# Kernel tuning notes

Hardware: AMD Instinct MI355X
Metric: run time of the kernel (lower is better)

The kernel has to match this reference:

```python
import jax, jax.numpy as jnp
import numpy as np

B, S, D, F, E, K = 2, 1024, 2048, 1024, 8, 2


def setup_inputs() -> dict:
    key = jax.random.key(0)
    ks = jax.random.split(key, 5)
    scale_x = 0.02
    return {
        "x": jax.random.normal(ks[0], (B, S, D), dtype=jnp.float32),
        "w_router": jax.random.normal(ks[1], (E, D), dtype=jnp.float32) * scale_x,
        "w_gate": jax.random.normal(ks[2], (E, F, D), dtype=jnp.float32) * scale_x,
        "w_up": jax.random.normal(ks[3], (E, F, D), dtype=jnp.float32) * scale_x,
        "w_down": jax.random.normal(ks[4], (E, D, F), dtype=jnp.float32) * scale_x,
        "top_k": K,
    }


def reference(x, w_router, w_gate, w_up, w_down, top_k):
    # Router: logits [B,S,E] -> top-k indices + softmax over top-k logits (fp32)
    logits = jnp.einsum("bsd,ed->bse", x, w_router)
    top_logits, top_idx = jax.lax.top_k(logits, top_k)          # [B,S,K]
    gates = jax.nn.softmax(top_logits.astype(jnp.float32), axis=-1)
    # SwitchGLU: per-expert gated MLP. Compute all experts densely, then gather
    # the selected expert output per token (reference-faithful math).
    h = jax.nn.silu(jnp.einsum("bsd,efd->besf", x, w_gate)) * jnp.einsum(
        "bsd,efd->besf", x, w_up
    )                                                            # [B,E,S,F]
    out_all = jnp.einsum("besf,edf->bsed", h, w_down)            # [B,S,E,D]
    y = jnp.take_along_axis(out_all, top_idx[..., None], axis=2)  # [B,S,K,D]
    return (y * gates[..., None].astype(y.dtype)).sum(axis=-2)   # [B,S,D]
```

## Files before the change

### kernel.cpp

```cpp
#include <hip/hip_runtime.h>
#include <hip/hip_bf16.h>

#define T_TOK 2048
#define DIM   2048
#define FFN   1024
#define NE    8

typedef __attribute__((ext_vector_type(8))) short bf16x8;
typedef __attribute__((ext_vector_type(4))) float f32x4;

__device__ __forceinline__ unsigned short f2bf(float f) {
  __hip_bfloat16 h = __float2bfloat16(f);
  return __builtin_bit_cast(unsigned short, h);
}

__device__ __forceinline__ void gload_lds16(const unsigned short* g, unsigned short* l) {
  __builtin_amdgcn_global_load_lds(
      (const __attribute__((address_space(1))) void*)g,
      (__attribute__((address_space(3))) void*)l, 16, 0, 0);
}

#define XN4 (T_TOK * DIM / 4)
#define WN4 (NE * FFN * DIM / 4)
__global__ void cvt_all(const float* __restrict__ x, const float* __restrict__ wg,
                        const float* __restrict__ wu, const float* __restrict__ wd,
                        unsigned short* __restrict__ xb, unsigned short* __restrict__ wgb,
                        unsigned short* __restrict__ wub, unsigned short* __restrict__ wdb) {
  long i = (long)blockIdx.x * blockDim.x + threadIdx.x;
  long stride = (long)gridDim.x * blockDim.x;
  const long TOTAL = (long)XN4 + 3L * WN4;
  for (; i < TOTAL; i += stride) {
    const float4* src; ushort4* dst; long j;
    if (i < XN4) {
      src = reinterpret_cast<const float4*>(x); dst = reinterpret_cast<ushort4*>(xb); j = i;
    } else {
      long k = i - XN4; int seg = (int)(k >> 22); j = k & (WN4 - 1);
      src = reinterpret_cast<const float4*>(seg == 0 ? wg : (seg == 1 ? wu : wd));
      dst = reinterpret_cast<ushort4*>(seg == 0 ? wgb : (seg == 1 ? wub : wdb));
    }
    float4 v = src[j];
    ushort4 o;
    o.x = f2bf(v.x); o.y = f2bf(v.y); o.z = f2bf(v.z); o.w = f2bf(v.w);
    dst[j] = o;
  }
}

__global__ __launch_bounds__(256) void router_topk(
    const float* __restrict__ x, const float* __restrict__ wr,
    int* __restrict__ top_i, float* __restrict__ top_g) {
  int t = blockIdx.x * 4 + (threadIdx.x >> 6);
  int lane = threadIdx.x & 63;
  const float4* xr = reinterpret_cast<const float4*>(x) + (size_t)t * (DIM / 4);
  const float4* wrv = reinterpret_cast<const float4*>(wr);
  float acc[NE];
#pragma unroll
  for (int e = 0; e < NE; ++e) acc[e] = 0.f;
#pragma unroll
  for (int it = 0; it < DIM / 4 / 64; ++it) {
    int d4 = it * 64 + lane;
    float4 xv = xr[d4];
#pragma unroll
    for (int e = 0; e < NE; ++e) {
      float4 wv = wrv[e * (DIM / 4) + d4];
      acc[e] += xv.x * wv.x + xv.y * wv.y + xv.z * wv.z + xv.w * wv.w;
    }
  }
#pragma unroll
  for (int off = 32; off > 0; off >>= 1) {
#pragma unroll
    for (int e = 0; e < NE; ++e) acc[e] += __shfl_xor(acc[e], off, 64);
  }
  if (lane == 0) {
    int i0 = 0; float m0 = acc[0];
#pragma unroll
    for (int e = 1; e < NE; ++e) if (acc[e] > m0) { m0 = acc[e]; i0 = e; }
    int i1 = -1; float m1 = -3.4e38f;
#pragma unroll
    for (int e = 0; e < NE; ++e) if (e != i0 && acc[e] > m1) { m1 = acc[e]; i1 = e; }
    float tv = expf(m1 - m0);
    float den = 1.f + tv;
    top_i[t * 2 + 0] = i0; top_i[t * 2 + 1] = i1;
    top_g[t * 2 + 0] = 1.f / den; top_g[t * 2 + 1] = tv / den;
  }
}

__global__ void count_offsets(const int* __restrict__ top_i,
                              int* __restrict__ offs, int* __restrict__ cursor) {
  __shared__ int cnt[NE];
  if (threadIdx.x < NE) cnt[threadIdx.x] = 0;
  __syncthreads();
  for (int i = threadIdx.x; i < T_TOK * 2; i += blockDim.x) atomicAdd(&cnt[top_i[i]], 1);
  __syncthreads();
  if (threadIdx.x == 0) {
    int s = 0;
    for (int e = 0; e < NE; ++e) { offs[e] = s; cursor[e] = s; s += cnt[e]; }
    offs[NE] = s;
  }
}

__global__ void scatter_tokens(const int* __restrict__ top_i, const float* __restrict__ top_g,
                               int* __restrict__ cursor, int* __restrict__ tok_list,
                               float* __restrict__ gate_lst, int* __restrict__ slot_lst) {
  int t = blockIdx.x * blockDim.x + threadIdx.x;
  if (t >= T_TOK) return;
#pragma unroll
  for (int s = 0; s < 2; ++s) {
    int e = top_i[t * 2 + s];
    int p = atomicAdd(&cursor[e], 1);
    tok_list[p] = t;
    gate_lst[p] = top_g[t * 2 + s];
    slot_lst[p] = s;
  }
}

__global__ __launch_bounds__(256, 4) void gateup_gemm(
    const unsigned short* __restrict__ xb, const unsigned short* __restrict__ wgb,
    const unsigned short* __restrict__ wub, const int* __restrict__ tok_list,
    const int* __restrict__ offs, unsigned short* __restrict__ hbuf) {
  const int e = blockIdx.z;
  const int row0 = offs[e];
  const int n_e = offs[e + 1] - row0;
  const int mt = blockIdx.y;
  if (mt * 64 >= n_e) return;
  const int nt = blockIdx.x;

  __shared__ unsigned short As[64 * 64];
  __shared__ unsigned short Bg[64 * 64];
  __shared__ unsigned short Bu[64 * 64];

  const int tid = threadIdx.x;
  const int wid = tid >> 6;
  const int lane = tid & 63;

  const int gchunk = (((lane & 7) ^ ((lane >> 3) & 7)) << 3);

  const unsigned short* gA[2];
  int lAoff[2];
#pragma unroll
  for (int p = 0; p < 2; ++p) {
    int rt = wid * 16 + p * 8 + (lane >> 3);
    int ar = mt * 64 + rt; if (ar >= n_e) ar = n_e - 1;
    gA[p] = xb + (size_t)tok_list[row0 + ar] * DIM + gchunk;
    lAoff[p] = (wid * 16 + p * 8) * 64;
  }
  const size_t wbase = (size_t)e * FFN * DIM + (size_t)(nt * 64) * DIM;
  const unsigned short* gG[2];
  const unsigned short* gU[2];
  int lBoff[2];
#pragma unroll
  for (int p = 0; p < 2; ++p) {
    int rt = wid * 16 + p * 8 + (lane >> 3);
    gG[p] = wgb + wbase + (size_t)rt * DIM + gchunk;
    gU[p] = wub + wbase + (size_t)rt * DIM + gchunk;
    lBoff[p] = (wid * 16 + p * 8) * 64;
  }

  f32x4 accg[2][2];
  f32x4 accu[2][2];
#pragma unroll
  for (int i = 0; i < 2; ++i)
#pragma unroll
    for (int j = 0; j < 2; ++j) {
      accg[i][j] = (f32x4){0.f, 0.f, 0.f, 0.f};
      accu[i][j] = (f32x4){0.f, 0.f, 0.f, 0.f};
    }

  const int warow = (wid >> 1) * 32;
  const int wacol = (wid & 1) * 32;
  const int frow = lane & 15;
  const int eo0 = ((((lane >> 4)) ^ (lane & 7)) << 3);
  const int eo1 = (((4 + (lane >> 4)) ^ (lane & 7)) << 3);

  for (int k0 = 0; k0 < DIM; k0 += 64) {
#pragma unroll
    for (int p = 0; p < 2; ++p) {
      gload_lds16(gA[p] + k0, &As[lAoff[p]]);
      gload_lds16(gG[p] + k0, &Bg[lBoff[p]]);
      gload_lds16(gU[p] + k0, &Bu[lBoff[p]]);
    }
    __syncthreads();
#pragma unroll
    for (int kk = 0; kk < 2; ++kk) {
      const int eo = kk ? eo1 : eo0;
      bf16x8 af[2], bg[2], bu[2];
#pragma unroll
      for (int i = 0; i < 2; ++i)
        af[i] = *reinterpret_cast<const bf16x8*>(&As[(warow + i * 16 + frow) * 64 + eo]);
#pragma unroll
      for (int j = 0; j < 2; ++j) {
        bg[j] = *reinterpret_cast<const bf16x8*>(&Bg[(wacol + j * 16 + frow) * 64 + eo]);
        bu[j] = *reinterpret_cast<const bf16x8*>(&Bu[(wacol + j * 16 + frow) * 64 + eo]);
      }
#pragma unroll
      for (int i = 0; i < 2; ++i)
#pragma unroll
        for (int j = 0; j < 2; ++j) {
          accg[i][j] = __builtin_amdgcn_mfma_f32_16x16x32_bf16(af[i], bg[j], accg[i][j], 0, 0, 0);
          accu[i][j] = __builtin_amdgcn_mfma_f32_16x16x32_bf16(af[i], bu[j], accu[i][j], 0, 0, 0);
        }
    }
    __syncthreads();
  }

#pragma unroll
  for (int i = 0; i < 2; ++i) {
#pragma unroll
    for (int jj = 0; jj < 4; ++jj) {
      int r = mt * 64 + warow + i * 16 + (lane >> 4) * 4 + jj;
      if (r < n_e) {
#pragma unroll
        for (int j = 0; j < 2; ++j) {
          float g = accg[i][j][jj];
          float u = accu[i][j][jj];
          float h = (g / (1.f + __expf(-g))) * u;
          int f = nt * 64 + wacol + j * 16 + (lane & 15);
          hbuf[(size_t)(row0 + r) * FFN + f] = f2bf(h);
        }
      }
    }
  }
}

__global__ __launch_bounds__(256, 4) void down_gemm(
    const unsigned short* __restrict__ hbuf, const unsigned short* __restrict__ wdb,
    const int* __restrict__ tok_list, const float* __restrict__ gate_lst,
    const int* __restrict__ slot_lst, const int* __restrict__ offs,
    float* __restrict__ yslots) {
  const int e = blockIdx.z;
  const int row0 = offs[e];
  const int n_e = offs[e + 1] - row0;
  const int mt = blockIdx.y;
  if (mt * 64 >= n_e) return;
  const int nt = blockIdx.x;

  __shared__ unsigned short As[64 * 64];
  __shared__ unsigned short Bs[128 * 64];

  const int tid = threadIdx.x;
  const int wid = tid >> 6;
  const int lane = tid & 63;

  const int gchunk = (((lane & 7) ^ ((lane >> 3) & 7)) << 3);

  const unsigned short* gA[2];
  int lAoff[2];
#pragma unroll
  for (int p = 0; p < 2; ++p) {
    int rt = wid * 16 + p * 8 + (lane >> 3);
    int ar = mt * 64 + rt; if (ar >= n_e) ar = n_e - 1;
    gA[p] = hbuf + (size_t)(row0 + ar) * FFN + gchunk;
    lAoff[p] = (wid * 16 + p * 8) * 64;
  }
  const unsigned short* gB[4];
  int lBoff[4];
#pragma unroll
  for (int p = 0; p < 4; ++p) {
    int rt = wid * 32 + p * 8 + (lane >> 3);
    gB[p] = wdb + ((size_t)e * DIM + nt * 128 + rt) * FFN + gchunk;
    lBoff[p] = (wid * 32 + p * 8) * 64;
  }

  f32x4 acc[2][4];
#pragma unroll
  for (int i = 0; i < 2; ++i)
#pragma unroll
    for (int j = 0; j < 4; ++j) acc[i][j] = (f32x4){0.f, 0.f, 0.f, 0.f};

  const int warow = (wid >> 1) * 32;
  const int wacol = (wid & 1) * 64;
  const int frow = lane & 15;
  const int eo0 = ((((lane >> 4)) ^ (lane & 7)) << 3);
  const int eo1 = (((4 + (lane >> 4)) ^ (lane & 7)) << 3);

  for (int k0 = 0; k0 < FFN; k0 += 64) {
#pragma unroll
    for (int p = 0; p < 2; ++p) gload_lds16(gA[p] + k0, &As[lAoff[p]]);
#pragma unroll
    for (int p = 0; p < 4; ++p) gload_lds16(gB[p] + k0, &Bs[lBoff[p]]);
    __syncthreads();
#pragma unroll
    for (int kk = 0; kk < 2; ++kk) {
      const int eo = kk ? eo1 : eo0;
      bf16x8 af[2], bf[4];
#pragma unroll
      for (int i = 0; i < 2; ++i)
        af[i] = *reinterpret_cast<const bf16x8*>(&As[(warow + i * 16 + frow) * 64 + eo]);
#pragma unroll
      for (int j = 0; j < 4; ++j)
        bf[j] = *reinterpret_cast<const bf16x8*>(&Bs[(wacol + j * 16 + frow) * 64 + eo]);
#pragma unroll
      for (int i = 0; i < 2; ++i)
#pragma unroll
        for (int j = 0; j < 4; ++j)
          acc[i][j] = __builtin_amdgcn_mfma_f32_16x16x32_bf16(af[i], bf[j], acc[i][j], 0, 0, 0);
    }
    __syncthreads();
  }

#pragma unroll
  for (int i = 0; i < 2; ++i) {
#pragma unroll
    for (int jj = 0; jj < 4; ++jj) {
      int r = mt * 64 + warow + i * 16 + (lane >> 4) * 4 + jj;
      if (r < n_e) {
        int tk = tok_list[row0 + r];
        float gt = gate_lst[row0 + r];
        int sl = slot_lst[row0 + r];
        float* yrow = yslots + ((size_t)sl * T_TOK + tk) * DIM;
#pragma unroll
        for (int j = 0; j < 4; ++j) {
          int d = nt * 128 + wacol + j * 16 + (lane & 15);
          yrow[d] = gt * acc[i][j][jj];
        }
      }
    }
  }
}

__global__ void combine(const float* __restrict__ y, float* __restrict__ out) {
  int i = blockIdx.x * blockDim.x + threadIdx.x;
  int stride = gridDim.x * blockDim.x;
  const float4* y0 = reinterpret_cast<const float4*>(y);
  const float4* y1 = reinterpret_cast<const float4*>(y + (size_t)T_TOK * DIM);
  float4* o = reinterpret_cast<float4*>(out);
  for (; i < T_TOK * DIM / 4; i += stride) {
    float4 a = y0[i], b = y1[i];
    float4 r;
    r.x = a.x + b.x; r.y = a.y + b.y; r.z = a.z + b.z; r.w = a.w + b.w;
    o[i] = r;
  }
}

extern "C" void kernel_launch(void* const* d_in, const int* in_sizes, int n_in,
                              void* d_out, int out_size, void* d_ws, size_t ws_size,
                              hipStream_t stream) {
  const float* x = (const float*)d_in[0];
  const float* wr = (const float*)d_in[1];
  const float* wg = (const float*)d_in[2];
  const float* wu = (const float*)d_in[3];
  const float* wd = (const float*)d_in[4];
  float* out = (float*)d_out;

  char* ws = (char*)d_ws;
  size_t off = 0;
  auto alloc = [&](size_t bytes) {
    char* p = ws + off;
    off += (bytes + 255) & ~(size_t)255;
    return p;
  };
  unsigned short* xb   = (unsigned short*)alloc((size_t)T_TOK * DIM * 2);
  unsigned short* wgb  = (unsigned short*)alloc((size_t)NE * FFN * DIM * 2);
  unsigned short* wub  = (unsigned short*)alloc((size_t)NE * FFN * DIM * 2);
  unsigned short* wdb  = (unsigned short*)alloc((size_t)NE * DIM * FFN * 2);
  unsigned short* hbuf = (unsigned short*)alloc((size_t)T_TOK * 2 * FFN * 2);
  float* yslots        = (float*)alloc((size_t)2 * T_TOK * DIM * 4);
  int* top_i     = (int*)alloc(T_TOK * 2 * 4);
  float* top_g   = (float*)alloc(T_TOK * 2 * 4);
  int* tok_list  = (int*)alloc(T_TOK * 2 * 4);
  float* gate_lst = (float*)alloc(T_TOK * 2 * 4);
  int* slot_lst  = (int*)alloc(T_TOK * 2 * 4);
  int* offs      = (int*)alloc(64);
  int* cursor    = (int*)alloc(64);
  if (off > ws_size) return;

  cvt_all<<<4096, 256, 0, stream>>>(x, wg, wu, wd, xb, wgb, wub, wdb);
  router_topk<<<T_TOK / 4, 256, 0, stream>>>(x, wr, top_i, top_g);
  count_offsets<<<1, 256, 0, stream>>>(top_i, offs, cursor);
  scatter_tokens<<<(T_TOK + 255) / 256, 256, 0, stream>>>(top_i, top_g, cursor, tok_list,
                                                          gate_lst, slot_lst);
  gateup_gemm<<<dim3(FFN / 64, 32, NE), 256, 0, stream>>>(xb, wgb, wub, tok_list, offs, hbuf);
  down_gemm<<<dim3(DIM / 128, 32, NE), 256, 0, stream>>>(hbuf, wdb, tok_list, gate_lst,
                                                         slot_lst, offs, yslots);
  combine<<<2048, 256, 0, stream>>>(yslots, out);
}
```

Baseline: 199.8 us.

## Overlap down-proj weight conversion with gate/up GEMM and widen fp32-to-bf16 stores

Replaces the single fused conversion kernel with per-tensor conversion kernels that write 8 bf16 values per thread per step. The conversion of w_down is moved into extra blocks of the gate/up GEMM grid, so it runs at the same time as the GEMM instead of before it. This aims to hide part of the memory-bound weight conversion behind compute. The risk is that the extra blocks compete with GEMM blocks for bandwidth and CU slots.

After: 221.6 us. 1.11x slower.

```diff
diff --git a/kernel.cpp b/kernel.cpp
--- a/kernel.cpp
+++ b/kernel.cpp
@@ -7,6 +7,7 @@
 #define NE    8
 
 typedef __attribute__((ext_vector_type(8))) short bf16x8;
+typedef __attribute__((ext_vector_type(8))) unsigned short u16x8;
 typedef __attribute__((ext_vector_type(4))) float f32x4;
 
 __device__ __forceinline__ unsigned short f2bf(float f) {
@@ -20,28 +21,25 @@
       (__attribute__((address_space(3))) void*)l, 16, 0, 0);
 }
 
-#define XN4 (T_TOK * DIM / 4)
-#define WN4 (NE * FFN * DIM / 4)
-__global__ void cvt_all(const float* __restrict__ x, const float* __restrict__ wg,
-                        const float* __restrict__ wu, const float* __restrict__ wd,
-                        unsigned short* __restrict__ xb, unsigned short* __restrict__ wgb,
-                        unsigned short* __restrict__ wub, unsigned short* __restrict__ wdb) {
-  long i = (long)blockIdx.x * blockDim.x + threadIdx.x;
-  long stride = (long)gridDim.x * blockDim.x;
-  const long TOTAL = (long)XN4 + 3L * WN4;
-  for (; i < TOTAL; i += stride) {
-    const float4* src; ushort4* dst; long j;
-    if (i < XN4) {
-      src = reinterpret_cast<const float4*>(x); dst = reinterpret_cast<ushort4*>(xb); j = i;
-    } else {
-      long k = i - XN4; int seg = (int)(k >> 22); j = k & (WN4 - 1);
-      src = reinterpret_cast<const float4*>(seg == 0 ? wg : (seg == 1 ? wu : wd));
-      dst = reinterpret_cast<ushort4*>(seg == 0 ? wgb : (seg == 1 ? wub : wdb));
-    }
-    float4 v = src[j];
-    ushort4 o;
-    o.x = f2bf(v.x); o.y = f2bf(v.y); o.z = f2bf(v.z); o.w = f2bf(v.w);
-    dst[j] = o;
+__device__ __forceinline__ u16x8 cvt8(float4 a, float4 b) {
+  u16x8 o;
+  o[0] = f2bf(a.x); o[1] = f2bf(a.y); o[2] = f2bf(a.z); o[3] = f2bf(a.w);
+  o[4] = f2bf(b.x); o[5] = f2bf(b.y); o[6] = f2bf(b.z); o[7] = f2bf(b.w);
+  return o;
+}
+
+__global__ __launch_bounds__(256) void cvt4(const float* __restrict__ src,
+                                            unsigned short* __restrict__ dst) {
+  const int tid = blockIdx.x * 256 + threadIdx.x;
+  const int nthreads = gridDim.x * 256;
+  const float4* s = reinterpret_cast<const float4*>(src);
+  u16x8* d = reinterpret_cast<u16x8*>(dst);
+#pragma unroll
+  for (int g = 0; g < 4; ++g) {
+    long grp = (long)g * nthreads + tid;
+    float4 a = s[grp * 2];
+    float4 b = s[grp * 2 + 1];
+    d[grp] = cvt8(a, b);
   }
 }
 
@@ -116,7 +114,22 @@
 __global__ __launch_bounds__(256, 4) void gateup_gemm(
     const unsigned short* __restrict__ xb, const unsigned short* __restrict__ wgb,
     const unsigned short* __restrict__ wub, const int* __restrict__ tok_list,
-    const int* __restrict__ offs, unsigned short* __restrict__ hbuf) {
+    const int* __restrict__ offs, unsigned short* __restrict__ hbuf,
+    const float* __restrict__ wd_f32, unsigned short* __restrict__ wdb) {
+  if (blockIdx.x >= FFN / 64) {
+    int cb = (blockIdx.x - FFN / 64) + 4 * (blockIdx.y + 32 * blockIdx.z);
+    int t = cb * 256 + threadIdx.x;
+    const float4* s = reinterpret_cast<const float4*>(wd_f32);
+    u16x8* d = reinterpret_cast<u16x8*>(wdb);
+#pragma unroll
+    for (int g = 0; g < 8; ++g) {
+      long grp = (long)g * 262144 + t;
+      float4 a = s[grp * 2];
+      float4 b = s[grp * 2 + 1];
+      d[grp] = cvt8(a, b);
+    }
+    return;
+  }
   const int e = blockIdx.z;
   const int row0 = offs[e];
   const int n_e = offs[e + 1] - row0;
@@ -363,12 +376,15 @@
   int* cursor    = (int*)alloc(64);
   if (off > ws_size) return;
 
-  cvt_all<<<4096, 256, 0, stream>>>(x, wg, wu, wd, xb, wgb, wub, wdb);
+  cvt4<<<512, 256, 0, stream>>>(x, xb);
+  cvt4<<<2048, 256, 0, stream>>>(wg, wgb);
+  cvt4<<<2048, 256, 0, stream>>>(wu, wub);
   router_topk<<<T_TOK / 4, 256, 0, stream>>>(x, wr, top_i, top_g);
   count_offsets<<<1, 256, 0, stream>>>(top_i, offs, cursor);
   scatter_tokens<<<(T_TOK + 255) / 256, 256, 0, stream>>>(top_i, top_g, cursor, tok_list,
                                                           gate_lst, slot_lst);
-  gateup_gemm<<<dim3(FFN / 64, 32, NE), 256, 0, stream>>>(xb, wgb, wub, tok_list, offs, hbuf);
+  gateup_gemm<<<dim3(FFN / 64 + 4, 32, NE), 256, 0, stream>>>(xb, wgb, wub, tok_list, offs,
+                                                              hbuf, wd, wdb);
   down_gemm<<<dim3(DIM / 128, 32, NE), 256, 0, stream>>>(hbuf, wdb, tok_list, gate_lst,
                                                          slot_lst, offs, yslots);
   combine<<<2048, 256, 0, stream>>>(yslots, out);
```

## Fuse x bf16 conversion into router, atomic-accumulate down output, drop combine

Applied to the files above, without the earlier changes.

The activation fp32-to-bf16 conversion moves into the router kernel, which already reads x, and weight conversion becomes its own kernel with a fixed per-block layout. The down GEMM now atomically adds gated results straight into a zeroed output, so the 32 MB two-slot scratch buffer, the slot list and the combine kernel all go away. This cuts global memory traffic and one launch. In exchange it adds a zeroing pass and float atomics, which make the summation order of the two expert contributions nondeterministic.

Measured after the change: 211.8 us. 6.0% more time.

```diff
diff --git a/kernel.cpp b/kernel.cpp
--- a/kernel.cpp
+++ b/kernel.cpp
@@ -20,38 +20,44 @@
       (__attribute__((address_space(3))) void*)l, 16, 0, 0);
 }
 
-#define XN4 (T_TOK * DIM / 4)
-#define WN4 (NE * FFN * DIM / 4)
-__global__ void cvt_all(const float* __restrict__ x, const float* __restrict__ wg,
-                        const float* __restrict__ wu, const float* __restrict__ wd,
-                        unsigned short* __restrict__ xb, unsigned short* __restrict__ wgb,
-                        unsigned short* __restrict__ wub, unsigned short* __restrict__ wdb) {
-  long i = (long)blockIdx.x * blockDim.x + threadIdx.x;
-  long stride = (long)gridDim.x * blockDim.x;
-  const long TOTAL = (long)XN4 + 3L * WN4;
-  for (; i < TOTAL; i += stride) {
-    const float4* src; ushort4* dst; long j;
-    if (i < XN4) {
-      src = reinterpret_cast<const float4*>(x); dst = reinterpret_cast<ushort4*>(xb); j = i;
-    } else {
-      long k = i - XN4; int seg = (int)(k >> 22); j = k & (WN4 - 1);
-      src = reinterpret_cast<const float4*>(seg == 0 ? wg : (seg == 1 ? wu : wd));
-      dst = reinterpret_cast<ushort4*>(seg == 0 ? wgb : (seg == 1 ? wub : wdb));
-    }
-    float4 v = src[j];
+__global__ void zero_out(float4* __restrict__ o, int n4) {
+  int i = blockIdx.x * blockDim.x + threadIdx.x;
+  int stride = gridDim.x * blockDim.x;
+  float4 z = {0.f, 0.f, 0.f, 0.f};
+  for (; i < n4; i += stride) o[i] = z;
+}
+
+__global__ __launch_bounds__(256) void cvt_w(
+    const float* __restrict__ wg, const float* __restrict__ wu, const float* __restrict__ wd,
+    unsigned short* __restrict__ wgb, unsigned short* __restrict__ wub,
+    unsigned short* __restrict__ wdb) {
+  int b = blockIdx.x;
+  const float* src; unsigned short* dst;
+  if (b < 4096)       { src = wg; dst = wgb; }
+  else if (b < 8192)  { src = wu; dst = wub; b -= 4096; }
+  else                { src = wd; dst = wdb; b -= 8192; }
+  const float4* s = reinterpret_cast<const float4*>(src);
+  ushort4* d = reinterpret_cast<ushort4*>(dst);
+  long base = (long)b * 1024 + threadIdx.x;
+#pragma unroll
+  for (int g = 0; g < 4; ++g) {
+    long i = base + g * 256;
+    float4 v = s[i];
     ushort4 o;
     o.x = f2bf(v.x); o.y = f2bf(v.y); o.z = f2bf(v.z); o.w = f2bf(v.w);
-    dst[j] = o;
+    d[i] = o;
   }
 }
 
 __global__ __launch_bounds__(256) void router_topk(
     const float* __restrict__ x, const float* __restrict__ wr,
-    int* __restrict__ top_i, float* __restrict__ top_g) {
+    int* __restrict__ top_i, float* __restrict__ top_g,
+    unsigned short* __restrict__ xb) {
   int t = blockIdx.x * 4 + (threadIdx.x >> 6);
   int lane = threadIdx.x & 63;
   const float4* xr = reinterpret_cast<const float4*>(x) + (size_t)t * (DIM / 4);
   const float4* wrv = reinterpret_cast<const float4*>(wr);
+  ushort4* xbr = reinterpret_cast<ushort4*>(xb + (size_t)t * DIM);
   float acc[NE];
 #pragma unroll
   for (int e = 0; e < NE; ++e) acc[e] = 0.f;
@@ -59,6 +65,9 @@
   for (int it = 0; it < DIM / 4 / 64; ++it) {
     int d4 = it * 64 + lane;
     float4 xv = xr[d4];
+    ushort4 o;
+    o.x = f2bf(xv.x); o.y = f2bf(xv.y); o.z = f2bf(xv.z); o.w = f2bf(xv.w);
+    xbr[d4] = o;
 #pragma unroll
     for (int e = 0; e < NE; ++e) {
       float4 wv = wrv[e * (DIM / 4) + d4];
@@ -100,7 +109,7 @@
 
 __global__ void scatter_tokens(const int* __restrict__ top_i, const float* __restrict__ top_g,
                                int* __restrict__ cursor, int* __restrict__ tok_list,
-                               float* __restrict__ gate_lst, int* __restrict__ slot_lst) {
+                               float* __restrict__ gate_lst) {
   int t = blockIdx.x * blockDim.x + threadIdx.x;
   if (t >= T_TOK) return;
 #pragma unroll
@@ -109,7 +118,6 @@
     int p = atomicAdd(&cursor[e], 1);
     tok_list[p] = t;
     gate_lst[p] = top_g[t * 2 + s];
-    slot_lst[p] = s;
   }
 }
 
@@ -224,8 +232,7 @@
 __global__ __launch_bounds__(256, 4) void down_gemm(
     const unsigned short* __restrict__ hbuf, const unsigned short* __restrict__ wdb,
     const int* __restrict__ tok_list, const float* __restrict__ gate_lst,
-    const int* __restrict__ slot_lst, const int* __restrict__ offs,
-    float* __restrict__ yslots) {
+    const int* __restrict__ offs, float* __restrict__ out) {
   const int e = blockIdx.z;
   const int row0 = offs[e];
   const int n_e = offs[e + 1] - row0;
@@ -305,29 +312,14 @@
       if (r < n_e) {
         int tk = tok_list[row0 + r];
         float gt = gate_lst[row0 + r];
-        int sl = slot_lst[row0 + r];
-        float* yrow = yslots + ((size_t)sl * T_TOK + tk) * DIM;
+        float* yrow = out + (size_t)tk * DIM;
 #pragma unroll
         for (int j = 0; j < 4; ++j) {
           int d = nt * 128 + wacol + j * 16 + (lane & 15);
-          yrow[d] = gt * acc[i][j][jj];
+          atomicAdd(&yrow[d], gt * acc[i][j][jj]);
         }
       }
     }
-  }
-}
-
-__global__ void combine(const float* __restrict__ y, float* __restrict__ out) {
-  int i = blockIdx.x * blockDim.x + threadIdx.x;
-  int stride = gridDim.x * blockDim.x;
-  const float4* y0 = reinterpret_cast<const float4*>(y);
-  const float4* y1 = reinterpret_cast<const float4*>(y + (size_t)T_TOK * DIM);
-  float4* o = reinterpret_cast<float4*>(out);
-  for (; i < T_TOK * DIM / 4; i += stride) {
-    float4 a = y0[i], b = y1[i];
-    float4 r;
-    r.x = a.x + b.x; r.y = a.y + b.y; r.z = a.z + b.z; r.w = a.w + b.w;
-    o[i] = r;
   }
 }
 
@@ -353,23 +345,21 @@
   unsigned short* wub  = (unsigned short*)alloc((size_t)NE * FFN * DIM * 2);
   unsigned short* wdb  = (unsigned short*)alloc((size_t)NE * DIM * FFN * 2);
   unsigned short* hbuf = (unsigned short*)alloc((size_t)T_TOK * 2 * FFN * 2);
-  float* yslots        = (float*)alloc((size_t)2 * T_TOK * DIM * 4);
   int* top_i     = (int*)alloc(T_TOK * 2 * 4);
   float* top_g   = (float*)alloc(T_TOK * 2 * 4);
   int* tok_list  = (int*)alloc(T_TOK * 2 * 4);
   float* gate_lst = (float*)alloc(T_TOK * 2 * 4);
-  int* slot_lst  = (int*)alloc(T_TOK * 2 * 4);
   int* offs      = (int*)alloc(64);
   int* cursor    = (int*)alloc(64);
   if (off > ws_size) return;
 
-  cvt_all<<<4096, 256, 0, stream>>>(x, wg, wu, wd, xb, wgb, wub, wdb);
-  router_topk<<<T_TOK / 4, 256, 0, stream>>>(x, wr, top_i, top_g);
+  zero_out<<<1024, 256, 0, stream>>>((float4*)out, T_TOK * DIM / 4);
+  cvt_w<<<12288, 256, 0, stream>>>(wg, wu, wd, wgb, wub, wdb);
+  router_topk<<<T_TOK / 4, 256, 0, stream>>>(x, wr, top_i, top_g, xb);
   count_offsets<<<1, 256, 0, stream>>>(top_i, offs, cursor);
   scatter_tokens<<<(T_TOK + 255) / 256, 256, 0, stream>>>(top_i, top_g, cursor, tok_list,
-                                                          gate_lst, slot_lst);
+                                                          gate_lst);
   gateup_gemm<<<dim3(FFN / 64, 32, NE), 256, 0, stream>>>(xb, wgb, wub, tok_list, offs, hbuf);
   down_gemm<<<dim3(DIM / 128, 32, NE), 256, 0, stream>>>(hbuf, wdb, tok_list, gate_lst,
-                                                         slot_lst, offs, yslots);
-  combine<<<2048, 256, 0, stream>>>(yslots, out);
-}
+                                                         offs, out);
+}
```
